# Kernel optimization log

Hardware: AMD Instinct MI355X
Metric: run time of the kernel (lower is better)

## Reference

```python
import jax, jax.numpy as jnp
import numpy as np
import itertools

N_OBJECTS = 6  # subsets of range(6), sizes 1..6 -> 63 subsets

def _subset_groups():
    # group subsets by length so each group runs as one batched LSTM
    groups = {}
    for m in range(1, N_OBJECTS + 1):
        for s in itertools.combinations(range(6), m):
            groups.setdefault(m, []).append(list(s))
    return [(m, np.asarray(v, dtype=np.int32)) for m, v in groups.items()]

SUBSET_GROUPS = _subset_groups()


def _lstm_final_h(x, W_ih, W_hh, b_ih, b_hh):
    """x: [B,T,D] -> final hidden state [B,H]. PyTorch gate order i,f,g,o."""
    H = W_hh.shape[1]
    B = x.shape[0]
    # precompute input projections for all timesteps: [B,T,4H]
    xz = jnp.einsum('btd,gd->btg', x, W_ih) + b_ih + b_hh

    def step(carry, xt):
        h, c = carry
        z = xt + h @ W_hh.T
        i, f, g, o = jnp.split(z, 4, axis=-1)
        c = jax.nn.sigmoid(f) * c + jax.nn.sigmoid(i) * jnp.tanh(g)
        h = jax.nn.sigmoid(o) * jnp.tanh(c)
        return (h, c), None

    h0 = jnp.zeros((B, H), x.dtype)
    (h, _), _ = jax.lax.scan(step, (h0, h0), jnp.swapaxes(xz, 0, 1))
    return h


def setup_inputs() -> dict:
    key = jax.random.key(0)
    ks = jax.random.split(key, 10)
    D, H, FC, A = 16, 128, 256, 10
    mb = 8192
    s = lambda k, shape, fan: jax.random.normal(k, shape, jnp.float32) * (1.0 / np.sqrt(fan))
    return {
        'x_input': jax.random.normal(ks[0], (mb, 6, D), jnp.float32),
        'W_ih': s(ks[1], (4 * H, D), D),
        'W_hh': s(ks[2], (4 * H, H), H),
        'b_ih': jnp.zeros((4 * H,), jnp.float32),
        'b_hh': jnp.zeros((4 * H,), jnp.float32),
        'fc1_W': s(ks[3], (FC, H), H),
        'fc1_b': jnp.zeros((FC,), jnp.float32),
        'fc2_W': s(ks[4], (A, FC), FC),
        'fc2_b': jnp.zeros((A,), jnp.float32),
    }


def reference(x_input, W_ih, W_hh, b_ih, b_hh, fc1_W, fc1_b, fc2_W, fc2_b):
    mb = x_input.shape[0]
    H = W_hh.shape[1]
    hs = []
    # subsets of the same length are batched into one LSTM pass (fused form of
    # the original 63-iteration python loop); aggregation is permutation-invariant
    for m, idx in SUBSET_GROUPS:
        nL = idx.shape[0]
        xg = x_input[:, idx, :]                       # [mb, nL, m, D] gather
        xg = xg.reshape(mb * nL, m, x_input.shape[-1])
        h = _lstm_final_h(xg, W_ih, W_hh, b_ih, b_hh)  # [mb*nL, H]
        hs.append(h.reshape(mb, nL, H))
    holder = jnp.concatenate(hs, axis=1)              # [mb, 63, H]
    x = jnp.max(holder, axis=1)                       # aggregate == 'max'
    x = jax.nn.relu(x @ fc1_W.T + fc1_b)
    x = x @ fc2_W.T + fc2_b
    return jax.nn.log_softmax(x, axis=-1)
```

## Files before the change

### kernel.cpp

```cpp
#include <hip/hip_runtime.h>
#include <hip/hip_bf16.h>

#define BLOCK   512
#define NSAMP   16
#define HDIM    128
#define DDIM    16
#define NOBJ    6
#define NSLOT   14

typedef __attribute__((ext_vector_type(8))) short bf16x8;
typedef __attribute__((ext_vector_type(4))) float f32x4;

constexpr int pc6(int m)  { int c = 0; for (int i = 0; i < 6; ++i) c += (m >> i) & 1; return c; }
constexpr int msb6(int m) { int b = -1; for (int i = 0; i < 6; ++i) if (m & (1 << i)) b = i; return b; }

struct PNode { int jo, ps, sl; bool bar; };
struct Plan2 { PNode nd[63]; int lvlStart[8]; };
constexpr Plan2 make_plan2() {
    Plan2 P{};
    int slotOf[64] = {};
    bool busy[NSLOT] = {};
    int k = 0;
    for (int d = 1; d <= 6; ++d) {
        P.lvlStart[d] = k;
        for (int M = 1; M < 64; ++M) {
            if (pc6(M) != d || msb6(M) != 5) continue;
            P.nd[k].jo = 5;
            P.nd[k].ps = (d == 1) ? -1 : slotOf[M & ~(1 << 5)];
            P.nd[k].sl = -1;
            P.nd[k].bar = false;
            ++k;
        }
        int pend[20] = {}; int np = 0;
        for (int M = 1; M < 64; ++M)
            if (pc6(M) == d && msb6(M) < 5) pend[np++] = M;
        int key[20] = {};
        for (int i = 0; i < np; ++i) {
            if (d == 1) { key[i] = 0; continue; }
            const int par = pend[i] & ~(1 << msb6(pend[i]));
            int c2 = 0;
            for (int j2 = 0; j2 < np; ++j2)
                if ((pend[j2] & ~(1 << msb6(pend[j2]))) == par) ++c2;
            key[i] = c2;
        }
        for (int a = 0; a < np; ++a)
            for (int b2 = a + 1; b2 < np; ++b2)
                if (key[b2] < key[a]) {
                    int tm = key[a]; key[a] = key[b2]; key[b2] = tm;
                    tm = pend[a]; pend[a] = pend[b2]; pend[b2] = tm;
                }
        bool placed[20] = {};
        int nplaced = 0;
        bool firstPhase = true;
        while (nplaced < np) {
            bool needBar = !firstPhase;
            bool any = false;
            for (int i = 0; i < np; ++i) {
                if (placed[i]) continue;
                int fs = -1;
                for (int s = 0; s < NSLOT; ++s) if (!busy[s]) { fs = s; break; }
                if (fs < 0) break;
                const int M = pend[i]; const int hi = msb6(M);
                busy[fs] = true; slotOf[M] = fs;
                P.nd[k].jo = hi;
                P.nd[k].ps = (d == 1) ? -1 : slotOf[M & ~(1 << hi)];
                P.nd[k].sl = fs;
                P.nd[k].bar = needBar; needBar = false;
                ++k; placed[i] = true; ++nplaced; any = true;
            }
            firstPhase = false;
            if (nplaced < np) {
                if (!any) break;
                for (int M = 1; M < 64; ++M) {
                    if (pc6(M) != d - 1 || msb6(M) >= 5) continue;
                    bool allp = true;
                    for (int i = 0; i < np; ++i)
                        if (!placed[i] &&
                            ((pend[i] & ~(1 << msb6(pend[i]))) == M)) allp = false;
                    if (allp) busy[slotOf[M]] = false;
                }
            }
        }
        for (int s = 0; s < NSLOT; ++s) busy[s] = false;
        for (int M = 1; M < 64; ++M)
            if (pc6(M) == d && msb6(M) < 5) busy[slotOf[M]] = true;
    }
    P.lvlStart[7] = k;
    return P;
}
constexpr Plan2 PL2 = make_plan2();
static_assert(PL2.lvlStart[7] == 63, "plan must cover all 63 nodes");

#define LOG2E   1.44269504f
#define TWOL2E  2.88539008f
#define SLOT_SH 2048

__device__ __forceinline__ unsigned short f2bf(float x) {
    union { float f; unsigned int u; } a; a.f = x;
    unsigned int r = (a.u + 0x7FFFu + ((a.u >> 16) & 1u)) >> 16;
    return (unsigned short)r;
}
__device__ __forceinline__ unsigned pk2(float a, float b) {
    union { __hip_bfloat162 h; unsigned u; } z;
    z.h = __float22bfloat162_rn(float2{a, b});
    return z.u;
}
__device__ __forceinline__ float bflo(unsigned p) {
    union { unsigned u; float f; } a; a.u = p << 16; return a.f;
}
__device__ __forceinline__ float bfhi(unsigned p) {
    union { unsigned u; float f; } a; a.u = p & 0xFFFF0000u; return a.f;
}


__global__ __launch_bounds__(BLOCK)
__attribute__((amdgpu_waves_per_eu(2, 4)))
void subset_lstm_skew_kernel(
    const float* __restrict__ x_input,
    const float* __restrict__ W_ih,
    const float* __restrict__ W_hh,
    const float* __restrict__ b_ih,
    const float* __restrict__ b_hh,
    const float* __restrict__ fc1_W,
    const float* __restrict__ fc1_b,
    const float* __restrict__ fc2_W,
    const float* __restrict__ fc2_b,
    float* __restrict__ out)
{
    __shared__ __align__(16) unsigned short hs [NSLOT * SLOT_SH];
    __shared__ __align__(16) unsigned short csb[NSLOT * SLOT_SH];
    __shared__ __align__(16) unsigned short xb[NOBJ * 4 * NSAMP * 8];
    float* s_maxh  = (float*)hs;
    float* s_fc1   = (float*)(hs + 4096);
    float* s_logit = (float*)xb;

    const int t      = threadIdx.x;
    const int w      = t >> 6;
    const int lane   = t & 63;
    const int quad   = lane >> 4;
    const int m16    = lane & 15;
    const int s_base = blockIdx.x * NSAMP;

    for (int idx = t; idx < NOBJ * 4 * NSAMP * 8; idx += BLOCK) {
        const int j = idx & 7, n = (idx >> 3) & 15, q = (idx >> 7) & 3, obj = idx >> 9;
        float v;
        if (q < 2) v = x_input[(s_base + n) * (NOBJ * DDIM) + obj * DDIM + q * 8 + j];
        else       v = (q == 2 && j == 0) ? 1.0f : 0.0f;
        xb[idx] = f2bf(v);
    }

    bf16x8 wf[4][5];
    #pragma unroll
    for (int g = 0; g < 4; ++g) {
        const float sc = (g == 2) ? TWOL2E : -LOG2E;
        const int grow = g * HDIM + w * 16 + m16;
        const float* whr = W_hh + grow * HDIM;
        const float* wir = W_ih + grow * DDIM;
        #pragma unroll
        for (int q = 0; q < 4; ++q) {
            union { unsigned short u[8]; bf16x8 v; } pk;
            #pragma unroll
            for (int j = 0; j < 8; ++j)
                pk.u[j] = f2bf(sc * whr[q * 32 + quad * 8 + j]);
            wf[g][q] = pk.v;
        }
        {
            union { unsigned short u[8]; bf16x8 v; } pk;
            #pragma unroll
            for (int j = 0; j < 8; ++j) {
                float v = 0.0f;
                if (quad < 2) v = sc * wir[quad * 8 + j];
                else if (quad == 2 && j == 0) v = sc * (b_ih[grow] + b_hh[grow]);
                pk.u[j] = f2bf(v);
            }
            wf[g][4] = pk.v;
        }
    }

    float mh[4] = {-1e30f, -1e30f, -1e30f, -1e30f};
    const int kslot = w * 2 + (quad >> 1);
    unsigned short* const c_lane = &csb[(((w * 4 + quad) * NSAMP) + m16) * 4];

    auto mfma_node = [&](f32x4 (&acc)[4], uint2& cpk, int jo, int ps) {
        cpk.x = 0u; cpk.y = 0u;
        if (ps >= 0) cpk = *(const uint2*)(c_lane + ps * SLOT_SH);
        {
            const bf16x8 bfx = *(const bf16x8*)&xb[((jo * 4 + quad) * NSAMP + m16) * 8];
            #pragma unroll
            for (int g = 0; g < 4; ++g)
                acc[g] = __builtin_amdgcn_mfma_f32_16x16x32_bf16(
                    wf[g][4], bfx, f32x4{0.f, 0.f, 0.f, 0.f}, 0, 0, 0);
        }
        if (ps >= 0) {
            #pragma unroll
            for (int q = 0; q < 4; ++q) {
                const bf16x8 bh = *(const bf16x8*)
                    &hs[((ps * 16 + q * 4 + quad) * NSAMP + m16) * 8];
                #pragma unroll
                for (int g = 0; g < 4; ++g)
                    acc[g] = __builtin_amdgcn_mfma_f32_16x16x32_bf16(
                        wf[g][q], bh, acc[g], 0, 0, 0);
            }
        }
    };

    auto pointwise_node = [&](const f32x4 (&acc)[4], uint2 cpk, int sl) {
        float cn4[4], hn4[4];
        #pragma unroll
        for (int r = 0; r < 4; ++r) {
            const unsigned p = (r < 2) ? cpk.x : cpk.y;
            const float cprev = (r & 1) ? bfhi(p) : bflo(p);
            const float u  = 1.0f + __builtin_amdgcn_exp2f(acc[0][r]);
            const float q  = 1.0f + __builtin_amdgcn_exp2f(acc[1][r]);
            const float v  = 1.0f + __builtin_amdgcn_exp2f(acc[2][r]);
            const float qo = 1.0f + __builtin_amdgcn_exp2f(acc[3][r]);
            const float uv  = u * v;
            const float num = fmaf(q, v - 2.0f, cprev * uv);
            const float cn  = num * __builtin_amdgcn_rcpf(q * uv);
            const float wt  = 1.0f + __builtin_amdgcn_exp2f(TWOL2E * cn);
            const float h   = (wt - 2.0f) * __builtin_amdgcn_rcpf(qo * wt);
            cn4[r] = cn; hn4[r] = h;
            mh[r] = fmaxf(mh[r], h);
        }
        if (sl >= 0) {
            uint2 cw; cw.x = pk2(cn4[0], cn4[1]); cw.y = pk2(cn4[2], cn4[3]);
            *(uint2*)(c_lane + sl * SLOT_SH) = cw;
            uint2 hw; hw.x = pk2(hn4[0], hn4[1]); hw.y = pk2(hn4[2], hn4[3]);
            *(uint2*)&hs[((sl * 16 + kslot) * NSAMP + m16) * 8 + (quad & 1) * 4] = hw;
        }
    };

    #pragma unroll
    for (int d = 1; d <= 6; ++d) {
        __syncthreads();
        const int kBeg = PL2.lvlStart[d];
        const int kEnd = PL2.lvlStart[d + 1];
        f32x4 accP[2][4];
        uint2 cpP[2];
        #pragma unroll
        for (int k = kBeg; k < kEnd; ++k) {
            const int par = (k - kBeg) & 1;
            if (PL2.nd[k].bar) __syncthreads();
            mfma_node(accP[par], cpP[par], PL2.nd[k].jo, PL2.nd[k].ps);
            if (k > kBeg)
                pointwise_node(accP[par ^ 1], cpP[par ^ 1], PL2.nd[k - 1].sl);
        }
        const int lpar = (kEnd - 1 - kBeg) & 1;
        pointwise_node(accP[lpar], cpP[lpar], PL2.nd[kEnd - 1].sl);
    }

    __syncthreads();
    {
        float4 v; v.x = mh[0]; v.y = mh[1]; v.z = mh[2]; v.w = mh[3];
        *(float4*)&s_maxh[m16 * HDIM + w * 16 + quad * 4] = v;
    }
    __syncthreads();

    {
        const int f  = t & 255;
        const int sh = t >> 8;
        float a1[8];
        #pragma unroll
        for (int s = 0; s < 8; ++s) a1[s] = fc1_b[f];
        for (int k4 = 0; k4 < HDIM / 4; ++k4) {
            const float4 wv = *(const float4*)&fc1_W[f * HDIM + k4 * 4];
            #pragma unroll
            for (int s = 0; s < 8; ++s) {
                const float4 h4 = *(const float4*)&s_maxh[(sh * 8 + s) * HDIM + k4 * 4];
                a1[s] += wv.x * h4.x + wv.y * h4.y + wv.z * h4.z + wv.w * h4.w;
            }
        }
        #pragma unroll
        for (int s = 0; s < 8; ++s)
            s_fc1[(sh * 8 + s) * 256 + f] = fmaxf(a1[s], 0.0f);
    }
    __syncthreads();

    if (t < NSAMP * 10) {
        const int s = t / 10, a = t % 10;
        float acc2 = fc2_b[a];
        for (int f4 = 0; f4 < 256 / 4; ++f4) {
            const float4 wv = *(const float4*)&fc2_W[a * 256 + f4 * 4];
            const float4 v  = *(const float4*)&s_fc1[s * 256 + f4 * 4];
            acc2 += wv.x * v.x + wv.y * v.y + wv.z * v.z + wv.w * v.w;
        }
        s_logit[s * 10 + a] = acc2;
    }
    __syncthreads();

    if (t < NSAMP) {
        float m = -1e30f;
        #pragma unroll
        for (int a = 0; a < 10; ++a) m = fmaxf(m, s_logit[t * 10 + a]);
        float sum = 0.0f;
        #pragma unroll
        for (int a = 0; a < 10; ++a) sum += __expf(s_logit[t * 10 + a] - m);
        const float lse = m + __logf(sum);
        #pragma unroll
        for (int a = 0; a < 10; ++a)
            out[(s_base + t) * 10 + a] = s_logit[t * 10 + a] - lse;
    }
}

extern "C" void kernel_launch(void* const* d_in, const int* in_sizes, int n_in,
                              void* d_out, int out_size, void* d_ws, size_t ws_size,
                              hipStream_t stream)
{
    (void)d_ws; (void)ws_size; (void)n_in; (void)out_size;

    const float* x   = (const float*)d_in[0];
    const float* Wih = (const float*)d_in[1];
    const float* Whh = (const float*)d_in[2];
    const float* bih = (const float*)d_in[3];
    const float* bhh = (const float*)d_in[4];
    const float* f1w = (const float*)d_in[5];
    const float* f1b = (const float*)d_in[6];
    const float* f2w = (const float*)d_in[7];
    const float* f2b = (const float*)d_in[8];

    const int mb = in_sizes[0] / (NOBJ * DDIM);
    dim3 grid(mb / NSAMP), block(BLOCK);
    subset_lstm_skew_kernel<<<grid, block, 0, stream>>>(
        x, Wih, Whh, bih, bhh, f1w, f1b, f2w, f2b, (float*)d_out);
}
```

Measured before the change: 194.6 us.

## Share parent recurrent projection across all children of each subset prefix

Restructures the subset-LSTM tree walk so that children are grouped by their parent prefix. The recurrent h@W_hh MFMA product is computed once per parent and reused for every child, which only adds its own input projection. This removes the redundant hidden-state MFMAs, cutting them from about 16 per node to 16 per parent group. In exchange it drops the two-node software pipelining of MFMA and pointwise work, increases the LDS slot count from 14 to 17, and changes where barriers fall.

```diff
diff --git a/kernel.cpp b/kernel.cpp
--- a/kernel.cpp
+++ b/kernel.cpp
@@ -6,7 +6,7 @@
 #define HDIM    128
 #define DDIM    16
 #define NOBJ    6
-#define NSLOT   14
+#define NSLOT   17
 
 typedef __attribute__((ext_vector_type(8))) short bf16x8;
 typedef __attribute__((ext_vector_type(4))) float f32x4;
@@ -14,82 +14,65 @@
 constexpr int pc6(int m)  { int c = 0; for (int i = 0; i < 6; ++i) c += (m >> i) & 1; return c; }
 constexpr int msb6(int m) { int b = -1; for (int i = 0; i < 6; ++i) if (m & (1 << i)) b = i; return b; }
 
-struct PNode { int jo, ps, sl; bool bar; };
-struct Plan2 { PNode nd[63]; int lvlStart[8]; };
-constexpr Plan2 make_plan2() {
-    Plan2 P{};
-    int slotOf[64] = {};
+struct GChild { int jo, sl; bool bar; };
+struct Plan3 {
+    int    gps [32];
+    int    gbeg[33];
+    GChild ch  [63];
+    int    lvlG[8];
+    bool   ok;
+};
+constexpr Plan3 make_plan3() {
+    Plan3 P{};
+    P.ok = true;
+    int  slotOf[64] = {};
     bool busy[NSLOT] = {};
-    int k = 0;
+    int  pendingFree[NSLOT] = {};
+    int  npend = 0;
+    int  g = 0, cidx = 0;
     for (int d = 1; d <= 6; ++d) {
-        P.lvlStart[d] = k;
-        for (int M = 1; M < 64; ++M) {
-            if (pc6(M) != d || msb6(M) != 5) continue;
-            P.nd[k].jo = 5;
-            P.nd[k].ps = (d == 1) ? -1 : slotOf[M & ~(1 << 5)];
-            P.nd[k].sl = -1;
-            P.nd[k].bar = false;
-            ++k;
-        }
-        int pend[20] = {}; int np = 0;
-        for (int M = 1; M < 64; ++M)
-            if (pc6(M) == d && msb6(M) < 5) pend[np++] = M;
-        int key[20] = {};
-        for (int i = 0; i < np; ++i) {
-            if (d == 1) { key[i] = 0; continue; }
-            const int par = pend[i] & ~(1 << msb6(pend[i]));
-            int c2 = 0;
-            for (int j2 = 0; j2 < np; ++j2)
-                if ((pend[j2] & ~(1 << msb6(pend[j2]))) == par) ++c2;
-            key[i] = c2;
-        }
-        for (int a = 0; a < np; ++a)
-            for (int b2 = a + 1; b2 < np; ++b2)
-                if (key[b2] < key[a]) {
-                    int tm = key[a]; key[a] = key[b2]; key[b2] = tm;
-                    tm = pend[a]; pend[a] = pend[b2]; pend[b2] = tm;
+        P.lvlG[d] = g;
+        for (int Pm = 0; Pm < 64; ++Pm) {
+            if (pc6(Pm) != d - 1) continue;
+            if (Pm != 0 && msb6(Pm) == 5) continue;
+            P.gps[g]  = (Pm == 0) ? -1 : slotOf[Pm];
+            P.gbeg[g] = cidx;
+            if (Pm != 0) pendingFree[npend++] = slotOf[Pm];
+            const int j0 = (Pm == 0) ? 0 : msb6(Pm) + 1;
+            for (int j = j0; j <= 5; ++j) {
+                const int M = Pm | (1 << j);
+                P.ch[cidx].jo  = j;
+                P.ch[cidx].bar = false;
+                int sl = -1;
+                if (j < 5) {
+                    int fs = -1;
+                    for (int s = 0; s < NSLOT; ++s) if (!busy[s]) { fs = s; break; }
+                    if (fs < 0) {
+                        P.ch[cidx].bar = true;
+                        for (int i = 0; i < npend; ++i) busy[pendingFree[i]] = false;
+                        npend = 0;
+                        for (int s = 0; s < NSLOT; ++s) if (!busy[s]) { fs = s; break; }
+                        if (fs < 0) P.ok = false;
+                    }
+                    if (fs >= 0) { busy[fs] = true; slotOf[M] = fs; sl = fs; }
                 }
-        bool placed[20] = {};
-        int nplaced = 0;
-        bool firstPhase = true;
-        while (nplaced < np) {
-            bool needBar = !firstPhase;
-            bool any = false;
-            for (int i = 0; i < np; ++i) {
-                if (placed[i]) continue;
-                int fs = -1;
-                for (int s = 0; s < NSLOT; ++s) if (!busy[s]) { fs = s; break; }
-                if (fs < 0) break;
-                const int M = pend[i]; const int hi = msb6(M);
-                busy[fs] = true; slotOf[M] = fs;
-                P.nd[k].jo = hi;
-                P.nd[k].ps = (d == 1) ? -1 : slotOf[M & ~(1 << hi)];
-                P.nd[k].sl = fs;
-                P.nd[k].bar = needBar; needBar = false;
-                ++k; placed[i] = true; ++nplaced; any = true;
-            }
-            firstPhase = false;
-            if (nplaced < np) {
-                if (!any) break;
-                for (int M = 1; M < 64; ++M) {
-                    if (pc6(M) != d - 1 || msb6(M) >= 5) continue;
-                    bool allp = true;
-                    for (int i = 0; i < np; ++i)
-                        if (!placed[i] &&
-                            ((pend[i] & ~(1 << msb6(pend[i]))) == M)) allp = false;
-                    if (allp) busy[slotOf[M]] = false;
-                }
-            }
-        }
-        for (int s = 0; s < NSLOT; ++s) busy[s] = false;
-        for (int M = 1; M < 64; ++M)
-            if (pc6(M) == d && msb6(M) < 5) busy[slotOf[M]] = true;
-    }
-    P.lvlStart[7] = k;
+                P.ch[cidx].sl = sl;
+                ++cidx;
+            }
+            ++g;
+        }
+        for (int i = 0; i < npend; ++i) busy[pendingFree[i]] = false;
+        npend = 0;
+    }
+    P.lvlG[7] = g;
+    P.gbeg[g] = cidx;
+    if (g != 32 || cidx != 63) P.ok = false;
     return P;
 }
-constexpr Plan2 PL2 = make_plan2();
-static_assert(PL2.lvlStart[7] == 63, "plan must cover all 63 nodes");
+constexpr Plan3 PL3 = make_plan3();
+static_assert(PL3.ok, "plan allocation failed");
+static_assert(PL3.lvlG[7] == 32, "32 groups expected");
+static_assert(PL3.gbeg[32] == 63, "63 children expected");
 
 #define LOG2E   1.44269504f
 #define TWOL2E  2.88539008f
@@ -181,29 +164,6 @@
     const int kslot = w * 2 + (quad >> 1);
     unsigned short* const c_lane = &csb[(((w * 4 + quad) * NSAMP) + m16) * 4];
 
-    auto mfma_node = [&](f32x4 (&acc)[4], uint2& cpk, int jo, int ps) {
-        cpk.x = 0u; cpk.y = 0u;
-        if (ps >= 0) cpk = *(const uint2*)(c_lane + ps * SLOT_SH);
-        {
-            const bf16x8 bfx = *(const bf16x8*)&xb[((jo * 4 + quad) * NSAMP + m16) * 8];
-            #pragma unroll
-            for (int g = 0; g < 4; ++g)
-                acc[g] = __builtin_amdgcn_mfma_f32_16x16x32_bf16(
-                    wf[g][4], bfx, f32x4{0.f, 0.f, 0.f, 0.f}, 0, 0, 0);
-        }
-        if (ps >= 0) {
-            #pragma unroll
-            for (int q = 0; q < 4; ++q) {
-                const bf16x8 bh = *(const bf16x8*)
-                    &hs[((ps * 16 + q * 4 + quad) * NSAMP + m16) * 8];
-                #pragma unroll
-                for (int g = 0; g < 4; ++g)
-                    acc[g] = __builtin_amdgcn_mfma_f32_16x16x32_bf16(
-                        wf[g][q], bh, acc[g], 0, 0, 0);
-            }
-        }
-    };
-
     auto pointwise_node = [&](const f32x4 (&acc)[4], uint2 cpk, int sl) {
         float cn4[4], hn4[4];
         #pragma unroll
@@ -233,20 +193,40 @@
     #pragma unroll
     for (int d = 1; d <= 6; ++d) {
         __syncthreads();
-        const int kBeg = PL2.lvlStart[d];
-        const int kEnd = PL2.lvlStart[d + 1];
-        f32x4 accP[2][4];
-        uint2 cpP[2];
-        #pragma unroll
-        for (int k = kBeg; k < kEnd; ++k) {
-            const int par = (k - kBeg) & 1;
-            if (PL2.nd[k].bar) __syncthreads();
-            mfma_node(accP[par], cpP[par], PL2.nd[k].jo, PL2.nd[k].ps);
-            if (k > kBeg)
-                pointwise_node(accP[par ^ 1], cpP[par ^ 1], PL2.nd[k - 1].sl);
-        }
-        const int lpar = (kEnd - 1 - kBeg) & 1;
-        pointwise_node(accP[lpar], cpP[lpar], PL2.nd[kEnd - 1].sl);
+        const int gBeg = PL3.lvlG[d];
+        const int gEnd = PL3.lvlG[d + 1];
+        #pragma unroll
+        for (int gi = gBeg; gi < gEnd; ++gi) {
+            const int ps = PL3.gps[gi];
+            f32x4 zh[4];
+            uint2 cpkP; cpkP.x = 0u; cpkP.y = 0u;
+            #pragma unroll
+            for (int g2 = 0; g2 < 4; ++g2) zh[g2] = f32x4{0.f, 0.f, 0.f, 0.f};
+            if (ps >= 0) {
+                cpkP = *(const uint2*)(c_lane + ps * SLOT_SH);
+                #pragma unroll
+                for (int q = 0; q < 4; ++q) {
+                    const bf16x8 bh = *(const bf16x8*)
+                        &hs[((ps * 16 + q * 4 + quad) * NSAMP + m16) * 8];
+                    #pragma unroll
+                    for (int g2 = 0; g2 < 4; ++g2)
+                        zh[g2] = __builtin_amdgcn_mfma_f32_16x16x32_bf16(
+                            wf[g2][q], bh, zh[g2], 0, 0, 0);
+                }
+            }
+            #pragma unroll
+            for (int ci = PL3.gbeg[gi]; ci < PL3.gbeg[gi + 1]; ++ci) {
+                if (PL3.ch[ci].bar) __syncthreads();
+                const bf16x8 bfx = *(const bf16x8*)
+                    &xb[((PL3.ch[ci].jo * 4 + quad) * NSAMP + m16) * 8];
+                f32x4 acc[4];
+                #pragma unroll
+                for (int g2 = 0; g2 < 4; ++g2)
+                    acc[g2] = __builtin_amdgcn_mfma_f32_16x16x32_bf16(
+                        wf[g2][4], bfx, zh[g2], 0, 0, 0);
+                pointwise_node(acc, cpkP, PL3.ch[ci].sl);
+            }
+        }
     }
 
     __syncthreads();
```

New measurement: 190.8 us. 2.0% less time.
